# Performance work log

Hardware: AMD Instinct MI355X
Metric: run time of the kernel (lower is better)

## Reference

```python
import jax, jax.numpy as jnp
import numpy as np

B = 8
D_IN = 1024
DIM = 256
H = 8
HD = DIM // H
SIZES = [32768, 8192, 2048]
NUM_LEVELS = 3


def setup_inputs() -> dict:
    key = jax.random.key(0)
    ks = jax.random.split(key, 12)
    def p(k, shape, scale=0.02):
        return jax.random.normal(k, shape, dtype=jnp.float32) * scale
    return {
        "x": jax.random.normal(ks[0], (B, D_IN), dtype=jnp.float32),
        "proj_w": p(ks[1], (NUM_LEVELS, DIM, D_IN)),
        "proj_b": p(ks[2], (NUM_LEVELS, DIM)),
        "mem0": p(ks[3], (SIZES[0], DIM), 0.05),
        "mem1": p(ks[4], (SIZES[1], DIM), 0.05),
        "mem2": p(ks[5], (SIZES[2], DIM), 0.05),
        "inw": p(ks[6], (NUM_LEVELS, 3 * DIM, DIM)),
        "inb": p(ks[7], (NUM_LEVELS, 3 * DIM)),
        "outw": p(ks[8], (NUM_LEVELS, DIM, DIM)),
        "outb": p(ks[9], (NUM_LEVELS, DIM)),
        "merg_w": p(ks[10], (D_IN, NUM_LEVELS * DIM)),
        "merg_b": p(ks[11], (D_IN,)),
    }


def _forward(x, proj_w, proj_b, mems, inw, inb, outw, outb, merg_w, merg_b):
    level_outputs = []
    updated_memories = []
    scale = 1.0 / np.sqrt(HD).astype(np.float32)
    for i in range(NUM_LEVELS):
        # per-level projection of x: [B, DIM]
        p = x @ proj_w[i].T + proj_b[i]
        mem = mems[i]  # [S, DIM] (shared across batch, prev_memories=None path)
        wq, wk, wv = inw[i][:DIM], inw[i][DIM:2 * DIM], inw[i][2 * DIM:]
        bq, bk, bv = inb[i][:DIM], inb[i][DIM:2 * DIM], inb[i][2 * DIM:]
        q = (p @ wq.T + bq).reshape(B, H, HD)            # [B, H, HD]
        k = (mem @ wk.T + bk).reshape(-1, H, HD)         # [S, H, HD]
        v = (mem @ wv.T + bv).reshape(-1, H, HD)         # [S, H, HD]
        # single-query attention over the memory bank
        scores = jnp.einsum("bhd,shd->bhs", q, k) * scale   # [B, H, S]
        attn = jax.nn.softmax(scores, axis=-1)
        o = jnp.einsum("bhs,shd->bhd", attn, v).reshape(B, DIM)
        o = o @ outw[i].T + outb[i]                      # attention out_proj
        level_outputs.append(o)
        # broadcast memory update: [B, S, DIM]
        updated_memories.append(mem[None, :, :] + p[:, None, :])
    combined = jnp.concatenate(level_outputs, axis=-1)  # [B, 3*DIM]
    out = combined @ merg_w.T + merg_b                   # [B, D_IN]
    return (out, updated_memories[0], updated_memories[1], updated_memories[2])


def reference(x, proj_w, proj_b, mem0, mem1, mem2, inw, inb, outw, outb, merg_w, merg_b):
    return _forward(x, proj_w, proj_b, (mem0, mem1, mem2), inw, inb, outw, outb, merg_w, merg_b)
```

## Files before the change

kernel.cpp:

```cpp
#include <hip/hip_runtime.h>
#include <math.h>

#define BATCH 8
#define SCALE 0.17677669529663687f

#define WS_P    0
#define WS_PP   6144
#define WS_QT   30720
#define WS_QBK  79872
#define WS_LVL  80064
#define WS_NUM  86208
#define WS_DEN  135360
#define WS_END  135552

#define UM0_F4 2048u
#define UM1_F4 16779264u
#define UM2_F4 20973568u

typedef float f4 __attribute__((ext_vector_type(4)));

__global__ __launch_bounds__(256) void kA1(const float* __restrict__ x,
                                           const float* __restrict__ proj_w,
                                           float* __restrict__ ws) {
    const int i = blockIdx.x, b = blockIdx.y, kk = blockIdx.z;
    const int t = threadIdx.x;
    __shared__ __align__(16) float xs[256];
    xs[t] = x[b * 1024 + kk * 256 + t];
    __syncthreads();
    const f4* w4 = reinterpret_cast<const f4*>(proj_w + (size_t)i * 262144 + (size_t)t * 1024 + kk * 256);
    const f4* x4 = reinterpret_cast<const f4*>(xs);
    float acc = 0.f;
    #pragma unroll 8
    for (int c = 0; c < 64; ++c) {
        f4 w = w4[c], xv = x4[c];
        acc += w.x * xv.x + w.y * xv.y + w.z * xv.z + w.w * xv.w;
    }
    ws[WS_PP + ((size_t)(i * 8 + b) * 256 + t) * 4 + kk] = acc;
}

__global__ __launch_bounds__(256) void kA2(const float* __restrict__ proj_b,
                                           const float* __restrict__ inw,
                                           const float* __restrict__ inb,
                                           float* __restrict__ ws) {
    const int i = blockIdx.x, b = blockIdx.y, t = threadIdx.x;
    __shared__ __align__(16) float ps[256];
    __shared__ __align__(16) float qs[256];
    float p = proj_b[i * 256 + t];
    #pragma unroll
    for (int kk = 0; kk < 4; ++kk) p += ws[WS_PP + ((size_t)(i * 8 + b) * 256 + t) * 4 + kk];
    ps[t] = p;
    ws[WS_P + i * 2048 + b * 256 + t] = p;
    __syncthreads();
    {
        const f4* w4 = reinterpret_cast<const f4*>(inw + (size_t)i * 196608 + (size_t)t * 256);
        const f4* p4 = reinterpret_cast<const f4*>(ps);
        float acc = inb[i * 768 + t];
        #pragma unroll 8
        for (int c = 0; c < 64; ++c) {
            f4 w = w4[c], pv = p4[c];
            acc += w.x * pv.x + w.y * pv.y + w.z * pv.z + w.w * pv.w;
        }
        qs[t] = acc;
    }
    __syncthreads();
    #pragma unroll 1
    for (int h = 0; h < 8; ++h) {
        const float* wk = inw + (size_t)i * 196608 + (size_t)(256 + h * 32) * 256;
        float acc = 0.f;
        #pragma unroll
        for (int d = 0; d < 32; ++d) acc += qs[h * 32 + d] * wk[(size_t)d * 256 + t];
        ws[WS_QT + i * 16384 + (b * 8 + h) * 256 + t] = acc * SCALE;
    }
    if (t < 8) {
        float acc = 0.f;
        #pragma unroll
        for (int d = 0; d < 32; ++d) acc += qs[t * 32 + d] * inb[i * 768 + 256 + t * 32 + d];
        ws[WS_QBK + i * 64 + b * 8 + t] = acc * SCALE;
    }
}

__global__ __launch_bounds__(512) void kF(const float* __restrict__ m0,
                                          const float* __restrict__ m1,
                                          const float* __restrict__ m2,
                                          float* __restrict__ ws,
                                          float* __restrict__ out) {
    const int bx = blockIdx.x;
    const int t = threadIdx.x;
    __shared__ __align__(16) f4 lds[2][1024];

    if (bx % 3 == 2) {
        const int aid = bx / 3;
        int lvl, s0;
        const float* mem;
        if (aid < 512)      { lvl = 0; s0 = aid << 6;         mem = m0; }
        else if (aid < 640) { lvl = 1; s0 = (aid - 512) << 6; mem = m1; }
        else                { lvl = 2; s0 = (aid - 640) << 6; mem = m2; }

        const int part = t & 15;
        const int grp = t >> 4;

        f4 qt[2][4];
        const f4* qtb = reinterpret_cast<const f4*>(ws + WS_QT + (size_t)lvl * 16384);
        #pragma unroll
        for (int bl = 0; bl < 2; ++bl)
            #pragma unroll
            for (int g = 0; g < 4; ++g)
                qt[bl][g] = qtb[(size_t)(grp * 2 + bl) * 64 + part + 16 * g];
        float qbk[2];
        #pragma unroll
        for (int bl = 0; bl < 2; ++bl) qbk[bl] = ws[WS_QBK + lvl * 64 + grp * 2 + bl];

        f4 nr[2][4];
        #pragma unroll
        for (int bl = 0; bl < 2; ++bl)
            #pragma unroll
            for (int g = 0; g < 4; ++g) nr[bl][g] = 0.f;
        float dn0 = 0.f, dn1 = 0.f;

        const f4* gm = reinterpret_cast<const f4*>(mem) + (size_t)s0 * 64;
        f4 st[2];
        #pragma unroll
        for (int k = 0; k < 2; ++k) st[k] = gm[t + 512 * k];
        #pragma unroll
        for (int k = 0; k < 2; ++k) lds[0][t + 512 * k] = st[k];
        __syncthreads();

        for (int tile = 0; tile < 4; ++tile) {
            if (tile < 3) {
                #pragma unroll
                for (int k = 0; k < 2; ++k) st[k] = gm[(tile + 1) * 1024 + t + 512 * k];
            }
            const f4* buf = lds[tile & 1];
            for (int r = 0; r < 16; ++r) {
                f4 m4[4];
                #pragma unroll
                for (int g = 0; g < 4; ++g) m4[g] = buf[r * 64 + part + 16 * g];
                float sc0 = 0.f, sc1 = 0.f;
                #pragma unroll
                for (int g = 0; g < 4; ++g) {
                    sc0 += qt[0][g].x * m4[g].x + qt[0][g].y * m4[g].y + qt[0][g].z * m4[g].z + qt[0][g].w * m4[g].w;
                    sc1 += qt[1][g].x * m4[g].x + qt[1][g].y * m4[g].y + qt[1][g].z * m4[g].z + qt[1][g].w * m4[g].w;
                }
                sc0 += __shfl_xor(sc0, 1); sc1 += __shfl_xor(sc1, 1);
                sc0 += __shfl_xor(sc0, 2); sc1 += __shfl_xor(sc1, 2);
                sc0 += __shfl_xor(sc0, 4); sc1 += __shfl_xor(sc1, 4);
                sc0 += __shfl_xor(sc0, 8); sc1 += __shfl_xor(sc1, 8);
                const float e0 = __expf(sc0 + qbk[0]);
                const float e1 = __expf(sc1 + qbk[1]);
                dn0 += e0; dn1 += e1;
                #pragma unroll
                for (int g = 0; g < 4; ++g) { nr[0][g] += e0 * m4[g]; nr[1][g] += e1 * m4[g]; }
            }
            if (tile < 3) {
                __syncthreads();
                #pragma unroll
                for (int k = 0; k < 2; ++k) lds[(tile + 1) & 1][t + 512 * k] = st[k];
                __syncthreads();
            }
        }

        #pragma unroll
        for (int bl = 0; bl < 2; ++bl) {
            const int bh = grp * 2 + bl;
            float* np = ws + WS_NUM + (size_t)lvl * 16384 + bh * 256 + part * 4;
            #pragma unroll
            for (int g = 0; g < 4; ++g) {
                #pragma unroll
                for (int j = 0; j < 4; ++j) atomicAdd(np + 64 * g + j, nr[bl][g][j]);
            }
            if (part == 0) atomicAdd(ws + WS_DEN + lvl * 64 + bh, bl == 0 ? dn0 : dn1);
        }
    } else {
        const int wid = bx - bx / 3;
        int lvl, logS;
        size_t row0, ob4;
        const float* mem;
        if (wid < 1024)      { lvl = 0; row0 = (size_t)wid << 5;          ob4 = UM0_F4; logS = 15; mem = m0; }
        else if (wid < 1280) { lvl = 1; row0 = (size_t)(wid - 1024) << 5; ob4 = UM1_F4; logS = 13; mem = m1; }
        else                 { lvl = 2; row0 = (size_t)(wid - 1280) << 5; ob4 = UM2_F4; logS = 11; mem = m2; }

        const int r = t >> 6;
        const int c4 = t & 63;
        f4 pr[8];
        #pragma unroll
        for (int b = 0; b < 8; ++b)
            pr[b] = reinterpret_cast<const f4*>(ws + WS_P + (size_t)lvl * 2048 + b * 256)[c4];

        const f4* mem4 = reinterpret_cast<const f4*>(mem);
        f4* o4 = reinterpret_cast<f4*>(out) + ob4;

        f4 mv[4];
        #pragma unroll
        for (int it = 0; it < 4; ++it)
            mv[it] = mem4[(row0 + it * 8 + r) * 64 + c4];
        #pragma unroll
        for (int it = 0; it < 4; ++it) {
            const size_t row = row0 + it * 8 + r;
            #pragma unroll
            for (int b = 0; b < 8; ++b)
                o4[((size_t)(b << logS) + row) * 64 + c4] = mv[it] + pr[b];
        }
    }
}

__global__ __launch_bounds__(1024) void kC(const float* __restrict__ inw,
                                           const float* __restrict__ inb,
                                           const float* __restrict__ outw,
                                           const float* __restrict__ outb,
                                           float* __restrict__ ws) {
    const int i = blockIdx.x, b = blockIdx.y, t = threadIdx.x;
    __shared__ __align__(16) float a[2048];
    __shared__ __align__(16) float ao[256];

    #pragma unroll
    for (int rep = 0; rep < 2; ++rep) {
        const int idx = rep * 1024 + t;
        a[idx] = ws[WS_NUM + i * 16384 + b * 2048 + idx] / ws[WS_DEN + i * 64 + b * 8 + (idx >> 8)];
    }
    __syncthreads();

    const int o = t >> 2, part = t & 3;
    {
        const f4* w4 = reinterpret_cast<const f4*>(inw + (size_t)i * 196608 + (size_t)(512 + o) * 256) + part * 16;
        const f4* a4 = reinterpret_cast<const f4*>(a + (o >> 5) * 256) + part * 16;
        float acc = 0.f;
        #pragma unroll
        for (int c = 0; c < 16; ++c) {
            f4 w = w4[c], av = a4[c];
            acc += w.x * av.x + w.y * av.y + w.z * av.z + w.w * av.w;
        }
        acc += __shfl_xor(acc, 1);
        acc += __shfl_xor(acc, 2);
        if (part == 0) ao[o] = acc + inb[i * 768 + 512 + o];
    }
    __syncthreads();
    {
        const f4* w4 = reinterpret_cast<const f4*>(outw + (size_t)i * 65536 + (size_t)o * 256) + part * 16;
        const f4* a4 = reinterpret_cast<const f4*>(ao) + part * 16;
        float acc = 0.f;
        #pragma unroll
        for (int c = 0; c < 16; ++c) {
            f4 w = w4[c], av = a4[c];
            acc += w.x * av.x + w.y * av.y + w.z * av.z + w.w * av.w;
        }
        acc += __shfl_xor(acc, 1);
        acc += __shfl_xor(acc, 2);
        if (part == 0) ws[WS_LVL + i * 2048 + b * 256 + o] = acc + outb[i * 256 + o];
    }
}

__global__ __launch_bounds__(1024) void kD(const float* __restrict__ merg_w,
                                           const float* __restrict__ merg_b,
                                           const float* __restrict__ ws,
                                           float* __restrict__ out) {
    const int b = blockIdx.x, quarter = blockIdx.y, t = threadIdx.x;
    __shared__ __align__(16) float comb[768];
    if (t < 768) comb[t] = ws[WS_LVL + (t >> 8) * 2048 + b * 256 + (t & 255)];
    __syncthreads();

    const int j = quarter * 256 + (t >> 2), part = t & 3;
    const f4* w4 = reinterpret_cast<const f4*>(merg_w + (size_t)j * 768) + part * 48;
    const f4* c4 = reinterpret_cast<const f4*>(comb) + part * 48;
    float acc = 0.f;
    #pragma unroll 8
    for (int c = 0; c < 48; ++c) {
        f4 w = w4[c], cv = c4[c];
        acc += w.x * cv.x + w.y * cv.y + w.z * cv.z + w.w * cv.w;
    }
    acc += __shfl_xor(acc, 1);
    acc += __shfl_xor(acc, 2);
    if (part == 0) out[b * 1024 + j] = acc + merg_b[j];
}

extern "C" void kernel_launch(void* const* d_in, const int* in_sizes, int n_in,
                              void* d_out, int out_size, void* d_ws, size_t ws_size,
                              hipStream_t stream) {
    const float* x      = (const float*)d_in[0];
    const float* proj_w = (const float*)d_in[1];
    const float* proj_b = (const float*)d_in[2];
    const float* mem0   = (const float*)d_in[3];
    const float* mem1   = (const float*)d_in[4];
    const float* mem2   = (const float*)d_in[5];
    const float* inw    = (const float*)d_in[6];
    const float* inb    = (const float*)d_in[7];
    const float* outw   = (const float*)d_in[8];
    const float* outb   = (const float*)d_in[9];
    const float* mw     = (const float*)d_in[10];
    const float* mb     = (const float*)d_in[11];
    float* out = (float*)d_out;
    float* ws  = (float*)d_ws;

    hipMemsetAsync(ws + WS_NUM, 0, (size_t)(WS_END - WS_NUM) * sizeof(float), stream);

    kA1<<<dim3(3, 8, 4), 256, 0, stream>>>(x, proj_w, ws);
    kA2<<<dim3(3, 8), 256, 0, stream>>>(proj_b, inw, inb, ws);
    kF<<<2016, 512, 0, stream>>>(mem0, mem1, mem2, ws, out);
    kC<<<dim3(3, 8), 1024, 0, stream>>>(inw, inb, outw, outb, ws);
    kD<<<dim3(8, 4), 1024, 0, stream>>>(mw, mb, ws, out);
}
```

Baseline: 323.9 us.

## Fuse prologue and epilogue kernels and coarsen attention blocks in fused kernel

Merges the two projection kernels into one 1024-thread kernel that reduces each split-K dot product with wave shuffles, and merges the out-projection and merge kernels into one kernel per batch that loops over levels. In the main kernel, each attention block now handles 256 memory rows instead of 64, giving 168 attention blocks placed before the memory-update blocks instead of interleaved with them. This cuts launch count, partial-sum traffic and the number of numerator atomics. In exchange it runs fewer, longer attention blocks that may load-balance worse against the update blocks, and the final kernel has only 8 blocks.

```diff
diff --git a/kernel.cpp b/kernel.cpp
--- a/kernel.cpp
+++ b/kernel.cpp
@@ -5,13 +5,11 @@
 #define SCALE 0.17677669529663687f
 
 #define WS_P    0
-#define WS_PP   6144
-#define WS_QT   30720
-#define WS_QBK  79872
-#define WS_LVL  80064
-#define WS_NUM  86208
-#define WS_DEN  135360
-#define WS_END  135552
+#define WS_QT   6144
+#define WS_QBK  55296
+#define WS_NUM  55488
+#define WS_DEN  104640
+#define WS_END  104832
 
 #define UM0_F4 2048u
 #define UM1_F4 16779264u
@@ -19,57 +17,64 @@
 
 typedef float f4 __attribute__((ext_vector_type(4)));
 
-__global__ __launch_bounds__(256) void kA1(const float* __restrict__ x,
+__global__ __launch_bounds__(1024) void kA(const float* __restrict__ x,
                                            const float* __restrict__ proj_w,
-                                           float* __restrict__ ws) {
-    const int i = blockIdx.x, b = blockIdx.y, kk = blockIdx.z;
-    const int t = threadIdx.x;
-    __shared__ __align__(16) float xs[256];
-    xs[t] = x[b * 1024 + kk * 256 + t];
-    __syncthreads();
-    const f4* w4 = reinterpret_cast<const f4*>(proj_w + (size_t)i * 262144 + (size_t)t * 1024 + kk * 256);
-    const f4* x4 = reinterpret_cast<const f4*>(xs);
-    float acc = 0.f;
-    #pragma unroll 8
-    for (int c = 0; c < 64; ++c) {
-        f4 w = w4[c], xv = x4[c];
-        acc += w.x * xv.x + w.y * xv.y + w.z * xv.z + w.w * xv.w;
-    }
-    ws[WS_PP + ((size_t)(i * 8 + b) * 256 + t) * 4 + kk] = acc;
-}
-
-__global__ __launch_bounds__(256) void kA2(const float* __restrict__ proj_b,
+                                           const float* __restrict__ proj_b,
                                            const float* __restrict__ inw,
                                            const float* __restrict__ inb,
                                            float* __restrict__ ws) {
     const int i = blockIdx.x, b = blockIdx.y, t = threadIdx.x;
+    __shared__ __align__(16) float xs[1024];
     __shared__ __align__(16) float ps[256];
     __shared__ __align__(16) float qs[256];
-    float p = proj_b[i * 256 + t];
-    #pragma unroll
-    for (int kk = 0; kk < 4; ++kk) p += ws[WS_PP + ((size_t)(i * 8 + b) * 256 + t) * 4 + kk];
-    ps[t] = p;
-    ws[WS_P + i * 2048 + b * 256 + t] = p;
+    const int o = t >> 2, part = t & 3;
+
+    xs[t] = x[b * 1024 + t];
     __syncthreads();
+
     {
-        const f4* w4 = reinterpret_cast<const f4*>(inw + (size_t)i * 196608 + (size_t)t * 256);
-        const f4* p4 = reinterpret_cast<const f4*>(ps);
-        float acc = inb[i * 768 + t];
+        const f4* w4 = reinterpret_cast<const f4*>(proj_w + (size_t)i * 262144 + (size_t)o * 1024) + part * 64;
+        const f4* x4 = reinterpret_cast<const f4*>(xs) + part * 64;
+        float acc = 0.f;
         #pragma unroll 8
         for (int c = 0; c < 64; ++c) {
+            f4 w = w4[c], xv = x4[c];
+            acc += w.x * xv.x + w.y * xv.y + w.z * xv.z + w.w * xv.w;
+        }
+        acc += __shfl_xor(acc, 1);
+        acc += __shfl_xor(acc, 2);
+        if (part == 0) {
+            const float p = acc + proj_b[i * 256 + o];
+            ps[o] = p;
+            ws[WS_P + i * 2048 + b * 256 + o] = p;
+        }
+    }
+    __syncthreads();
+
+    {
+        const f4* w4 = reinterpret_cast<const f4*>(inw + (size_t)i * 196608 + (size_t)o * 256) + part * 16;
+        const f4* p4 = reinterpret_cast<const f4*>(ps) + part * 16;
+        float acc = 0.f;
+        #pragma unroll
+        for (int c = 0; c < 16; ++c) {
             f4 w = w4[c], pv = p4[c];
             acc += w.x * pv.x + w.y * pv.y + w.z * pv.z + w.w * pv.w;
         }
-        qs[t] = acc;
+        acc += __shfl_xor(acc, 1);
+        acc += __shfl_xor(acc, 2);
+        if (part == 0) qs[o] = acc + inb[i * 768 + o];
     }
     __syncthreads();
-    #pragma unroll 1
-    for (int h = 0; h < 8; ++h) {
-        const float* wk = inw + (size_t)i * 196608 + (size_t)(256 + h * 32) * 256;
-        float acc = 0.f;
-        #pragma unroll
-        for (int d = 0; d < 32; ++d) acc += qs[h * 32 + d] * wk[(size_t)d * 256 + t];
-        ws[WS_QT + i * 16384 + (b * 8 + h) * 256 + t] = acc * SCALE;
+
+    #pragma unroll
+    for (int rep = 0; rep < 2; ++rep) {
+        const int idx = rep * 1024 + t;
+        const int h = idx >> 8, c = idx & 255;
+        const float* wk = inw + (size_t)i * 196608 + (size_t)(256 + h * 32) * 256 + c;
+        float acc = 0.f;
+        #pragma unroll
+        for (int d = 0; d < 32; ++d) acc += qs[h * 32 + d] * wk[(size_t)d * 256];
+        ws[WS_QT + i * 16384 + (b * 8 + h) * 256 + c] = acc * SCALE;
     }
     if (t < 8) {
         float acc = 0.f;
@@ -88,13 +93,13 @@
     const int t = threadIdx.x;
     __shared__ __align__(16) f4 lds[2][1024];
 
-    if (bx % 3 == 2) {
-        const int aid = bx / 3;
+    if (bx < 168) {
+        const int aid = bx;
         int lvl, s0;
         const float* mem;
-        if (aid < 512)      { lvl = 0; s0 = aid << 6;         mem = m0; }
-        else if (aid < 640) { lvl = 1; s0 = (aid - 512) << 6; mem = m1; }
-        else                { lvl = 2; s0 = (aid - 640) << 6; mem = m2; }
+        if (aid < 128)      { lvl = 0; s0 = aid << 8;         mem = m0; }
+        else if (aid < 160) { lvl = 1; s0 = (aid - 128) << 8; mem = m1; }
+        else                { lvl = 2; s0 = (aid - 160) << 8; mem = m2; }
 
         const int part = t & 15;
         const int grp = t >> 4;
@@ -125,10 +130,10 @@
         for (int k = 0; k < 2; ++k) lds[0][t + 512 * k] = st[k];
         __syncthreads();
 
-        for (int tile = 0; tile < 4; ++tile) {
-            if (tile < 3) {
-                #pragma unroll
-                for (int k = 0; k < 2; ++k) st[k] = gm[(tile + 1) * 1024 + t + 512 * k];
+        for (int tile = 0; tile < 16; ++tile) {
+            if (tile < 15) {
+                #pragma unroll
+                for (int k = 0; k < 2; ++k) st[k] = gm[(size_t)(tile + 1) * 1024 + t + 512 * k];
             }
             const f4* buf = lds[tile & 1];
             for (int r = 0; r < 16; ++r) {
@@ -151,7 +156,7 @@
                 #pragma unroll
                 for (int g = 0; g < 4; ++g) { nr[0][g] += e0 * m4[g]; nr[1][g] += e1 * m4[g]; }
             }
-            if (tile < 3) {
+            if (tile < 15) {
                 __syncthreads();
                 #pragma unroll
                 for (int k = 0; k < 2; ++k) lds[(tile + 1) & 1][t + 512 * k] = st[k];
@@ -171,7 +176,7 @@
             if (part == 0) atomicAdd(ws + WS_DEN + lvl * 64 + bh, bl == 0 ? dn0 : dn1);
         }
     } else {
-        const int wid = bx - bx / 3;
+        const int wid = bx - 168;
         int lvl, logS;
         size_t row0, ob4;
         const float* mem;
@@ -203,73 +208,72 @@
     }
 }
 
-__global__ __launch_bounds__(1024) void kC(const float* __restrict__ inw,
+__global__ __launch_bounds__(1024) void kE(const float* __restrict__ inw,
                                            const float* __restrict__ inb,
                                            const float* __restrict__ outw,
                                            const float* __restrict__ outb,
-                                           float* __restrict__ ws) {
-    const int i = blockIdx.x, b = blockIdx.y, t = threadIdx.x;
-    __shared__ __align__(16) float a[2048];
-    __shared__ __align__(16) float ao[256];
-
-    #pragma unroll
-    for (int rep = 0; rep < 2; ++rep) {
-        const int idx = rep * 1024 + t;
-        a[idx] = ws[WS_NUM + i * 16384 + b * 2048 + idx] / ws[WS_DEN + i * 64 + b * 8 + (idx >> 8)];
-    }
-    __syncthreads();
-
-    const int o = t >> 2, part = t & 3;
-    {
-        const f4* w4 = reinterpret_cast<const f4*>(inw + (size_t)i * 196608 + (size_t)(512 + o) * 256) + part * 16;
-        const f4* a4 = reinterpret_cast<const f4*>(a + (o >> 5) * 256) + part * 16;
-        float acc = 0.f;
-        #pragma unroll
-        for (int c = 0; c < 16; ++c) {
-            f4 w = w4[c], av = a4[c];
-            acc += w.x * av.x + w.y * av.y + w.z * av.z + w.w * av.w;
-        }
-        acc += __shfl_xor(acc, 1);
-        acc += __shfl_xor(acc, 2);
-        if (part == 0) ao[o] = acc + inb[i * 768 + 512 + o];
-    }
-    __syncthreads();
-    {
-        const f4* w4 = reinterpret_cast<const f4*>(outw + (size_t)i * 65536 + (size_t)o * 256) + part * 16;
-        const f4* a4 = reinterpret_cast<const f4*>(ao) + part * 16;
-        float acc = 0.f;
-        #pragma unroll
-        for (int c = 0; c < 16; ++c) {
-            f4 w = w4[c], av = a4[c];
-            acc += w.x * av.x + w.y * av.y + w.z * av.z + w.w * av.w;
-        }
-        acc += __shfl_xor(acc, 1);
-        acc += __shfl_xor(acc, 2);
-        if (part == 0) ws[WS_LVL + i * 2048 + b * 256 + o] = acc + outb[i * 256 + o];
-    }
-}
-
-__global__ __launch_bounds__(1024) void kD(const float* __restrict__ merg_w,
+                                           const float* __restrict__ merg_w,
                                            const float* __restrict__ merg_b,
                                            const float* __restrict__ ws,
                                            float* __restrict__ out) {
-    const int b = blockIdx.x, quarter = blockIdx.y, t = threadIdx.x;
+    const int b = blockIdx.x, t = threadIdx.x;
+    __shared__ __align__(16) float a[2048];
+    __shared__ __align__(16) float ao[256];
     __shared__ __align__(16) float comb[768];
-    if (t < 768) comb[t] = ws[WS_LVL + (t >> 8) * 2048 + b * 256 + (t & 255)];
-    __syncthreads();
-
-    const int j = quarter * 256 + (t >> 2), part = t & 3;
-    const f4* w4 = reinterpret_cast<const f4*>(merg_w + (size_t)j * 768) + part * 48;
-    const f4* c4 = reinterpret_cast<const f4*>(comb) + part * 48;
-    float acc = 0.f;
-    #pragma unroll 8
-    for (int c = 0; c < 48; ++c) {
-        f4 w = w4[c], cv = c4[c];
-        acc += w.x * cv.x + w.y * cv.y + w.z * cv.z + w.w * cv.w;
-    }
-    acc += __shfl_xor(acc, 1);
-    acc += __shfl_xor(acc, 2);
-    if (part == 0) out[b * 1024 + j] = acc + merg_b[j];
+    const int o = t >> 2, part = t & 3;
+
+    for (int i = 0; i < 3; ++i) {
+        #pragma unroll
+        for (int rep = 0; rep < 2; ++rep) {
+            const int idx = rep * 1024 + t;
+            a[idx] = ws[WS_NUM + i * 16384 + b * 2048 + idx] / ws[WS_DEN + i * 64 + b * 8 + (idx >> 8)];
+        }
+        __syncthreads();
+        {
+            const f4* w4 = reinterpret_cast<const f4*>(inw + (size_t)i * 196608 + (size_t)(512 + o) * 256) + part * 16;
+            const f4* a4 = reinterpret_cast<const f4*>(a + (o >> 5) * 256) + part * 16;
+            float acc = 0.f;
+            #pragma unroll
+            for (int c = 0; c < 16; ++c) {
+                f4 w = w4[c], av = a4[c];
+                acc += w.x * av.x + w.y * av.y + w.z * av.z + w.w * av.w;
+            }
+            acc += __shfl_xor(acc, 1);
+            acc += __shfl_xor(acc, 2);
+            if (part == 0) ao[o] = acc + inb[i * 768 + 512 + o];
+        }
+        __syncthreads();
+        {
+            const f4* w4 = reinterpret_cast<const f4*>(outw + (size_t)i * 65536 + (size_t)o * 256) + part * 16;
+            const f4* a4 = reinterpret_cast<const f4*>(ao) + part * 16;
+            float acc = 0.f;
+            #pragma unroll
+            for (int c = 0; c < 16; ++c) {
+                f4 w = w4[c], av = a4[c];
+                acc += w.x * av.x + w.y * av.y + w.z * av.z + w.w * av.w;
+            }
+            acc += __shfl_xor(acc, 1);
+            acc += __shfl_xor(acc, 2);
+            if (part == 0) comb[i * 256 + o] = acc + outb[i * 256 + o];
+        }
+        __syncthreads();
+    }
+
+    #pragma unroll 1
+    for (int quarter = 0; quarter < 4; ++quarter) {
+        const int j = quarter * 256 + o;
+        const f4* w4 = reinterpret_cast<const f4*>(merg_w + (size_t)j * 768) + part * 48;
+        const f4* c4 = reinterpret_cast<const f4*>(comb) + part * 48;
+        float acc = 0.f;
+        #pragma unroll 8
+        for (int c = 0; c < 48; ++c) {
+            f4 w = w4[c], cv = c4[c];
+            acc += w.x * cv.x + w.y * cv.y + w.z * cv.z + w.w * cv.w;
+        }
+        acc += __shfl_xor(acc, 1);
+        acc += __shfl_xor(acc, 2);
+        if (part == 0) out[b * 1024 + j] = acc + merg_b[j];
+    }
 }
 
 extern "C" void kernel_launch(void* const* d_in, const int* in_sizes, int n_in,
@@ -292,9 +296,7 @@
 
     hipMemsetAsync(ws + WS_NUM, 0, (size_t)(WS_END - WS_NUM) * sizeof(float), stream);
 
-    kA1<<<dim3(3, 8, 4), 256, 0, stream>>>(x, proj_w, ws);
-    kA2<<<dim3(3, 8), 256, 0, stream>>>(proj_b, inw, inb, ws);
-    kF<<<2016, 512, 0, stream>>>(mem0, mem1, mem2, ws, out);
-    kC<<<dim3(3, 8), 1024, 0, stream>>>(inw, inb, outw, outb, ws);
-    kD<<<dim3(8, 4), 1024, 0, stream>>>(mw, mb, ws, out);
+    kA<<<dim3(3, 8), 1024, 0, stream>>>(x, proj_w, proj_b, inw, inb, ws);
+    kF<<<1512, 512, 0, stream>>>(mem0, mem1, mem2, ws, out);
+    kE<<<8, 1024, 0, stream>>>(inw, inb, outw, outb, mw, mb, ws, out);
 }
```

New measurement: 369.9 us. 1.14x slower.

## Fold memset into kA1 and fuse kC into kF via last-block reduction

Applied to the files above, without the earlier changes.

Removes the separate hipMemsetAsync by having kA1 blocks zero the numerator, denominator and counter workspace. Eliminates the kC launch by having the last attention block (detected with an atomic counter) normalize the accumulated numerators and run the V-projection and out-projection for all 24 level/batch pairs. This saves two launches on the stream, but puts the serial tail work on a single 512-thread block, which may be slower than kC's 24 parallel blocks.

```diff
diff --git a/kernel.cpp b/kernel.cpp
--- a/kernel.cpp
+++ b/kernel.cpp
@@ -8,10 +8,12 @@
 #define WS_PP   6144
 #define WS_QT   30720
 #define WS_QBK  79872
-#define WS_LVL  80064
-#define WS_NUM  86208
-#define WS_DEN  135360
-#define WS_END  135552
+#define WS_NUM  80064
+#define WS_DEN  129216
+#define WS_CNT  129408
+#define WS_LVL  129412
+#define WS_END  135556
+#define WS_ZN   49345
 
 #define UM0_F4 2048u
 #define UM1_F4 16779264u
@@ -24,6 +26,10 @@
                                            float* __restrict__ ws) {
     const int i = blockIdx.x, b = blockIdx.y, kk = blockIdx.z;
     const int t = threadIdx.x;
+    {
+        const int bid = (i * 8 + b) * 4 + kk;
+        for (int k = bid * 256 + t; k < WS_ZN; k += 24576) ws[WS_NUM + k] = 0.f;
+    }
     __shared__ __align__(16) float xs[256];
     xs[t] = x[b * 1024 + kk * 256 + t];
     __syncthreads();
@@ -82,6 +88,10 @@
 __global__ __launch_bounds__(512) void kF(const float* __restrict__ m0,
                                           const float* __restrict__ m1,
                                           const float* __restrict__ m2,
+                                          const float* __restrict__ inw,
+                                          const float* __restrict__ inb,
+                                          const float* __restrict__ outw,
+                                          const float* __restrict__ outb,
                                           float* __restrict__ ws,
                                           float* __restrict__ out) {
     const int bx = blockIdx.x;
@@ -128,7 +138,7 @@
         for (int tile = 0; tile < 4; ++tile) {
             if (tile < 3) {
                 #pragma unroll
-                for (int k = 0; k < 2; ++k) st[k] = gm[(tile + 1) * 1024 + t + 512 * k];
+                for (int k = 0; k < 2; ++k) st[k] = gm[(size_t)(tile + 1) * 1024 + t + 512 * k];
             }
             const f4* buf = lds[tile & 1];
             for (int r = 0; r < 16; ++r) {
@@ -170,6 +180,59 @@
             }
             if (part == 0) atomicAdd(ws + WS_DEN + lvl * 64 + bh, bl == 0 ? dn0 : dn1);
         }
+
+        float* af  = reinterpret_cast<float*>(lds);
+        float* aof = af + 2048;
+        float* dsh = af + 2304;
+        unsigned int* lf = (unsigned int*)(af + 2312);
+        __syncthreads();
+        if (t == 0) {
+            unsigned int* cnt = (unsigned int*)(ws + WS_CNT);
+            *lf = (atomicAdd(cnt, 1u) == 671u) ? 1u : 0u;
+        }
+        __syncthreads();
+        if (*lf != 1u) return;
+
+        const int o = t >> 1, prt = t & 1;
+        for (int ib = 0; ib < 24; ++ib) {
+            const int i = ib >> 3, b = ib & 7;
+            if (t < 8) dsh[t] = atomicAdd(ws + WS_DEN + i * 64 + b * 8 + t, 0.f);
+            float raw[4];
+            #pragma unroll
+            for (int r = 0; r < 4; ++r)
+                raw[r] = atomicAdd(ws + WS_NUM + i * 16384 + b * 2048 + r * 512 + t, 0.f);
+            __syncthreads();
+            #pragma unroll
+            for (int r = 0; r < 4; ++r)
+                af[r * 512 + t] = raw[r] / dsh[(r * 512 + t) >> 8];
+            __syncthreads();
+            {
+                const f4* w4 = reinterpret_cast<const f4*>(inw + (size_t)i * 196608 + (size_t)(512 + o) * 256) + prt * 32;
+                const f4* a4 = reinterpret_cast<const f4*>(af + ((o >> 5) << 8)) + prt * 32;
+                float acc = 0.f;
+                #pragma unroll
+                for (int c = 0; c < 32; ++c) {
+                    f4 w = w4[c], av = a4[c];
+                    acc += w.x * av.x + w.y * av.y + w.z * av.z + w.w * av.w;
+                }
+                acc += __shfl_xor(acc, 1);
+                if (prt == 0) aof[o] = acc + inb[i * 768 + 512 + o];
+            }
+            __syncthreads();
+            {
+                const f4* w4 = reinterpret_cast<const f4*>(outw + (size_t)i * 65536 + (size_t)o * 256) + prt * 32;
+                const f4* a4 = reinterpret_cast<const f4*>(aof) + prt * 32;
+                float acc = 0.f;
+                #pragma unroll
+                for (int c = 0; c < 32; ++c) {
+                    f4 w = w4[c], av = a4[c];
+                    acc += w.x * av.x + w.y * av.y + w.z * av.z + w.w * av.w;
+                }
+                acc += __shfl_xor(acc, 1);
+                if (prt == 0) ws[WS_LVL + i * 2048 + b * 256 + o] = acc + outb[i * 256 + o];
+            }
+            __syncthreads();
+        }
     } else {
         const int wid = bx - bx / 3;
         int lvl, logS;
@@ -200,52 +263,6 @@
             for (int b = 0; b < 8; ++b)
                 o4[((size_t)(b << logS) + row) * 64 + c4] = mv[it] + pr[b];
         }
-    }
-}
-
-__global__ __launch_bounds__(1024) void kC(const float* __restrict__ inw,
-                                           const float* __restrict__ inb,
-                                           const float* __restrict__ outw,
-                                           const float* __restrict__ outb,
-                                           float* __restrict__ ws) {
-    const int i = blockIdx.x, b = blockIdx.y, t = threadIdx.x;
-    __shared__ __align__(16) float a[2048];
-    __shared__ __align__(16) float ao[256];
-
-    #pragma unroll
-    for (int rep = 0; rep < 2; ++rep) {
-        const int idx = rep * 1024 + t;
-        a[idx] = ws[WS_NUM + i * 16384 + b * 2048 + idx] / ws[WS_DEN + i * 64 + b * 8 + (idx >> 8)];
-    }
-    __syncthreads();
-
-    const int o = t >> 2, part = t & 3;
-    {
-        const f4* w4 = reinterpret_cast<const f4*>(inw + (size_t)i * 196608 + (size_t)(512 + o) * 256) + part * 16;
-        const f4* a4 = reinterpret_cast<const f4*>(a + (o >> 5) * 256) + part * 16;
-        float acc = 0.f;
-        #pragma unroll
-        for (int c = 0; c < 16; ++c) {
-            f4 w = w4[c], av = a4[c];
-            acc += w.x * av.x + w.y * av.y + w.z * av.z + w.w * av.w;
-        }
-        acc += __shfl_xor(acc, 1);
-        acc += __shfl_xor(acc, 2);
-        if (part == 0) ao[o] = acc + inb[i * 768 + 512 + o];
-    }
-    __syncthreads();
-    {
-        const f4* w4 = reinterpret_cast<const f4*>(outw + (size_t)i * 65536 + (size_t)o * 256) + part * 16;
-        const f4* a4 = reinterpret_cast<const f4*>(ao) + part * 16;
-        float acc = 0.f;
-        #pragma unroll
-        for (int c = 0; c < 16; ++c) {
-            f4 w = w4[c], av = a4[c];
-            acc += w.x * av.x + w.y * av.y + w.z * av.z + w.w * av.w;
-        }
-        acc += __shfl_xor(acc, 1);
-        acc += __shfl_xor(acc, 2);
-        if (part == 0) ws[WS_LVL + i * 2048 + b * 256 + o] = acc + outb[i * 256 + o];
     }
 }
 
@@ -290,11 +307,8 @@
     float* out = (float*)d_out;
     float* ws  = (float*)d_ws;
 
-    hipMemsetAsync(ws + WS_NUM, 0, (size_t)(WS_END - WS_NUM) * sizeof(float), stream);
-
     kA1<<<dim3(3, 8, 4), 256, 0, stream>>>(x, proj_w, ws);
     kA2<<<dim3(3, 8), 256, 0, stream>>>(proj_b, inw, inb, ws);
-    kF<<<2016, 512, 0, stream>>>(mem0, mem1, mem2, ws, out);
-    kC<<<dim3(3, 8), 1024, 0, stream>>>(inw, inb, outw, outb, ws);
+    kF<<<2016, 512, 0, stream>>>(mem0, mem1, mem2, inw, inb, outw, outb, ws, out);
     kD<<<dim3(8, 4), 1024, 0, stream>>>(mw, mb, ws, out);
 }
```

Result: slower. 674.8 us (+108.3%).
